# Kernel tuning notes

Hardware: AMD Instinct MI355X
Metric: run time of the kernel (lower is better)

## Reference

```python
import jax, jax.numpy as jnp
import numpy as np

SEQ_LEN = 168; PRED_LEN = 24; N_FEAT = 8; KERNEL = 25
N_QUBITS = 4; N_QLAYERS = 2; CONTEXT = 32; HIDDEN = 8; BATCH = 16384
LAG_POSITIONS = [1, 2, 3, 4, 5, 6, 23, 24, 25, 167, 168]
LAG_IDX = np.array([SEQ_LEN - l for l in LAG_POSITIONS if l <= SEQ_LEN])
N_LAGS = int(LAG_IDX.size)
PI = float(np.pi)


def _apply_1q(state, U, w):
    # apply 2x2 gate U (shared (2,2) or per-sample (B,2,2)) on wire w
    state = jnp.moveaxis(state, 1 + w, -1)
    if U.ndim == 2:
        state = jnp.einsum('ij,b...j->b...i', U, state)
    else:
        state = jnp.einsum('bij,b...j->b...i', U, state)
    return jnp.moveaxis(state, -1, 1 + w)


def _apply_cnot(state, c, t):
    ax_c, ax_t = 1 + c, 1 + t
    s0 = jax.lax.index_in_dim(state, 0, ax_c, keepdims=False)
    s1 = jax.lax.index_in_dim(state, 1, ax_c, keepdims=False)
    s1 = jnp.flip(s1, axis=ax_t - (1 if t > c else 0))
    return jnp.stack([s0, s1], axis=ax_c)


def _ry(theta):  # (B,) -> (B,2,2)
    c, s = jnp.cos(theta / 2), jnp.sin(theta / 2)
    return jnp.stack([jnp.stack([c, -s], -1), jnp.stack([s, c], -1)], -2).astype(jnp.complex64)


def _rot(w):  # w (3,): Rot(phi,theta,omega) = RZ(omega) RY(theta) RZ(phi)
    phi, theta, omega = w[0], w[1], w[2]
    c, s = jnp.cos(theta / 2), jnp.sin(theta / 2)
    ep = jnp.exp(-0.5j * (phi + omega))
    em = jnp.exp(0.5j * (phi - omega))
    return jnp.stack([jnp.stack([ep * c, -em * s]),
                      jnp.stack([jnp.conj(em) * s, jnp.conj(ep) * c])]).astype(jnp.complex64)


def _vqc(inputs, weights):
    # data re-uploading: [RY AngleEmbedding -> Rot per wire -> CNOT ring (range 1)] x N_QLAYERS
    # (StronglyEntanglingLayers is called with 1 layer per upload, so range is always 1)
    B = inputs.shape[0]
    state = jnp.zeros((B,) + (2,) * N_QUBITS, jnp.complex64)
    state = state.at[(slice(None),) + (0,) * N_QUBITS].set(1.0)
    for l in range(N_QLAYERS):
        for q in range(N_QUBITS):
            state = _apply_1q(state, _ry(inputs[:, q]), q)
        for q in range(N_QUBITS):
            state = _apply_1q(state, _rot(weights[l, q]), q)
        for q in range(N_QUBITS):
            state = _apply_cnot(state, q, (q + 1) % N_QUBITS)
    probs = state.real ** 2 + state.imag ** 2  # (B,2,2,2,2)
    zdiag = jnp.array([1.0, -1.0], jnp.float32)
    exps = []
    for q in range(N_QUBITS):
        other = tuple(a for a in range(1, N_QUBITS + 1) if a != 1 + q)
        exps.append(jnp.einsum('bq,q->b', probs.sum(other), zdiag))
    return jnp.stack(exps, axis=-1)  # (B, N_QUBITS)


def _decomp(x, decomp_w):
    # learnable moving-average decomposition (DLinear-style, per-feature softmax kernel, edge padding)
    pad = (KERNEL - 1) // 2
    w = jax.nn.softmax(decomp_w, axis=-1)  # (F,K)
    xp = jnp.pad(x, ((0, 0), (pad, KERNEL - 1 - pad), (0, 0)), mode='edge')
    xc = jnp.moveaxis(xp, 1, 2)  # (B,F,S+K-1)
    trend = jax.lax.conv_general_dilated(xc, w[:, None, :], (1,), 'VALID',
                                         feature_group_count=N_FEAT,
                                         dimension_numbers=('NCH', 'OIH', 'NCH'))
    trend = jnp.moveaxis(trend, 1, 2)  # (B,S,F)
    return x - trend, trend


def forward(x, decomp_w, trend_w, trend_b, seasonal_w, seasonal_b, h0_w, h0_b,
            ta_w, ta_b, sc_w, sc_b, crz_w, crz_b, cn_w, cn_b,
            vqc_r, vqc_u, vqc_c, expand_w, expand_b, mod_w, mod_b, fusion_alpha):
    seasonal, trend = _decomp(x, decomp_w)
    trend_out = jnp.einsum('bsf,ps->bpf', trend, trend_w) + trend_b[None, :, None]
    seasonal_base = jnp.einsum('bsf,ps->bpf', seasonal, seasonal_w) + seasonal_b[None, :, None]
    lag_vals = x[:, LAG_IDX, -1]  # (B, N_LAGS), demand is last feature
    h0 = jnp.tanh(lag_vals @ h0_w.T + h0_b)  # (B,H)
    ctx = jnp.einsum('bsf,cs->bfc', seasonal, ta_w) + ta_b  # (B,F,C)
    gru_in = jnp.tanh(ctx.reshape(x.shape[0], -1) @ sc_w.T + sc_b)  # (B,H)
    # single-step quantum GRU
    xh = jnp.concatenate([gru_in, h0], axis=1)  # (B,2H)
    rz_in = jnp.tanh(xh @ crz_w.T + crz_b) * PI  # r_in == z_in (same compress in source)
    r = jax.nn.sigmoid(_vqc(rz_in, vqc_r) @ expand_w.T + expand_b)
    z = jax.nn.sigmoid(_vqc(rz_in, vqc_u) @ expand_w.T + expand_b)
    n_in = jnp.tanh(jnp.concatenate([r * h0, gru_in], axis=1) @ cn_w.T + cn_b) * PI
    n = jnp.tanh(_vqc(n_in, vqc_c) @ expand_w.T + expand_b)
    h_new = (1 - z) * n + z * h0
    modulation = jnp.tanh(h_new @ mod_w.T + mod_b)  # (B,P)
    seasonal_out = seasonal_base * (1.0 + modulation[:, :, None])
    alpha = jax.nn.sigmoid(fusion_alpha)[0]
    return alpha * seasonal_out + (1 - alpha) * trend_out  # (B,P,F)


def setup_inputs() -> dict:
    key = jax.random.key(0)
    ks = iter(jax.random.split(key, 32))

    def lin(out_d, in_d):
        lim = 1.0 / np.sqrt(in_d)
        return (jax.random.uniform(next(ks), (out_d, in_d), jnp.float32, -lim, lim),
                jax.random.uniform(next(ks), (out_d,), jnp.float32, -lim, lim))

    trend_w, trend_b = lin(PRED_LEN, SEQ_LEN)
    seasonal_w, seasonal_b = lin(PRED_LEN, SEQ_LEN)
    h0_w, h0_b = lin(HIDDEN, N_LAGS)
    ta_w, ta_b = lin(CONTEXT, SEQ_LEN)
    sc_w, sc_b = lin(HIDDEN, N_FEAT * CONTEXT)
    crz_w, crz_b = lin(N_QUBITS, 2 * HIDDEN)
    cn_w, cn_b = lin(N_QUBITS, 2 * HIDDEN)
    expand_w, expand_b = lin(HIDDEN, N_QUBITS)
    mod_w, mod_b = lin(PRED_LEN, HIDDEN)
    return {
        'x': jax.random.normal(next(ks), (BATCH, SEQ_LEN, N_FEAT), jnp.float32),
        'decomp_w': 0.02 * jax.random.normal(next(ks), (N_FEAT, KERNEL), jnp.float32),
        'trend_w': trend_w, 'trend_b': trend_b,
        'seasonal_w': seasonal_w, 'seasonal_b': seasonal_b,
        'h0_w': h0_w, 'h0_b': h0_b,
        'ta_w': ta_w, 'ta_b': ta_b,
        'sc_w': sc_w, 'sc_b': sc_b,
        'crz_w': crz_w, 'crz_b': crz_b,
        'cn_w': cn_w, 'cn_b': cn_b,
        'vqc_r': jax.random.uniform(next(ks), (N_QLAYERS, N_QUBITS, 3), jnp.float32, 0.0, 2 * PI),
        'vqc_u': jax.random.uniform(next(ks), (N_QLAYERS, N_QUBITS, 3), jnp.float32, 0.0, 2 * PI),
        'vqc_c': jax.random.uniform(next(ks), (N_QLAYERS, N_QUBITS, 3), jnp.float32, 0.0, 2 * PI),
        'expand_w': expand_w, 'expand_b': expand_b,
        'mod_w': mod_w, 'mod_b': mod_b,
        'fusion_alpha': jnp.array([0.5], jnp.float32),
    }


def reference(x, decomp_w, trend_w, trend_b, seasonal_w, seasonal_b, h0_w, h0_b,
              ta_w, ta_b, sc_w, sc_b, crz_w, crz_b, cn_w, cn_b,
              vqc_r, vqc_u, vqc_c, expand_w, expand_b, mod_w, mod_b, fusion_alpha):
    return forward(x, decomp_w, trend_w, trend_b, seasonal_w, seasonal_b, h0_w, h0_b,
                   ta_w, ta_b, sc_w, sc_b, crz_w, crz_b, cn_w, cn_b,
                   vqc_r, vqc_u, vqc_c, expand_w, expand_b, mod_w, mod_b, fusion_alpha)
```

## Files before the change

### kernel.cpp

```cpp
#include <hip/hip_runtime.h>
#include <hip/hip_bf16.h>
#include <cmath>

#define SEQ   168
#define NF    8
#define PRED  24
#define HID   8
#define KTOT  1344
#define NSCH  6
#define PI_F  3.14159265358979323846f

#define WS_ROTC     256
#define WS_CGIN     512
#define WS_WT       1024
#define WS_IMG_BYTE 524288

typedef __attribute__((ext_vector_type(8))) short bf16x8;
typedef __attribute__((ext_vector_type(4))) float f32x4;

__device__ __forceinline__ float frcp(float x)  { return __builtin_amdgcn_rcpf(x); }
__device__ __forceinline__ float ftanh(float x) {
    float xc = fminf(fmaxf(x, -15.f), 15.f);
    float e  = __expf(2.f * xc);
    return (e - 1.f) * frcp(e + 1.f);
}
__device__ __forceinline__ float sigm(float x) { return frcp(1.f + __expf(-x)); }
__device__ __forceinline__ unsigned short f2bf(float f) {
    __hip_bfloat16 h = __float2bfloat16(f);
    return __builtin_bit_cast(unsigned short, h);
}
__device__ __forceinline__ unsigned pack2(float a, float b) {
    return (unsigned)f2bf(a) | ((unsigned)f2bf(b) << 16);
}

__global__ void k_compose(const float* __restrict__ decomp_w,
                          const float* __restrict__ trend_w,
                          const float* __restrict__ seasonal_w,
                          const float* __restrict__ ta_w,
                          float* __restrict__ Wt) {
    __shared__ float dwsh[NF * 25];
    int t = threadIdx.x;
    if (t < NF) {
        const float* row = decomp_w + t * 25;
        float m = row[0];
        for (int k = 1; k < 25; ++k) m = fmaxf(m, row[k]);
        float e[25]; float sum = 0.f;
        for (int k = 0; k < 25; ++k) { e[k] = expf(row[k] - m); sum += e[k]; }
        float inv = 1.f / sum;
        for (int k = 0; k < 25; ++k) dwsh[t * 25 + k] = e[k] * inv;
    }
    __syncthreads();
    int n = blockIdx.x * 256 + t;
    if (n >= SEQ * 640) return;
    int sx  = n / 640;
    int col = n % 640;
    int j = col >> 3;
    int f = col & 7;
    const float* dwf = dwsh + f * 25;
    const float* wsel;
    int isTrend = 0;
    if (j < 24)      { wsel = trend_w    + j        * SEQ; isTrend = 1; }
    else if (j < 48) { wsel = seasonal_w + (j - 24) * SEQ; }
    else             { wsel = ta_w       + (j - 48) * SEQ; }
    float acc = 0.f;
    if (sx == 0) {
        for (int s = 0; s <= 12; ++s) {
            float cw = 0.f;
            for (int k = 0; k <= 12 - s; ++k) cw += dwf[k];
            acc = fmaf(cw, wsel[s], acc);
        }
    } else if (sx == 167) {
        for (int s = 155; s < 168; ++s) {
            float cw = 0.f;
            for (int k = 179 - s; k < 25; ++k) cw += dwf[k];
            acc = fmaf(cw, wsel[s], acc);
        }
    } else {
        int lo = sx - 12; if (lo < 0) lo = 0;
        int hi = sx + 12; if (hi > 167) hi = 167;
        for (int s = lo; s <= hi; ++s) acc = fmaf(dwf[sx - s + 12], wsel[s], acc);
    }
    Wt[sx * 640 + col] = isTrend ? acc : (wsel[sx] - acc);
}

__global__ void k_img(const float* __restrict__ Wt, const float* __restrict__ sc_w,
                      const float* __restrict__ h0_w,
                      const float* __restrict__ vr, const float* __restrict__ vu,
                      const float* __restrict__ vc,
                      const float* __restrict__ sc_b, const float* __restrict__ ta_b,
                      float* __restrict__ rotc, float* __restrict__ cgin,
                      unsigned char* __restrict__ imgb) {
    int idx = blockIdx.x * 256 + threadIdx.x;
    if (idx < 12288) {
        int lane = idx & 63;
        int rest = idx >> 6;
        int ks = rest % 6;
        int fc = rest / 6;
        int cf = fc & 3, f = fc >> 2;
        int lr = lane & 15, lg = lane >> 4;
        unsigned short vals[8];
        #pragma unroll
        for (int e = 0; e < 8; ++e) {
            int k = ks * 32 + lg * 8 + e;
            float val = 0.f;
            if (k < SEQ) {
                if (cf < 3) {
                    int col = cf * 16 + lr;
                    val = Wt[k * 640 + (col & 1) * 192 + (col >> 1) * 8 + f];
                } else if (lr < 8) {
                    float a = 0.f;
                    for (int cc = 0; cc < 32; ++cc)
                        a = fmaf(sc_w[lr * 256 + f * 32 + cc], Wt[k * 640 + 384 + cc * 8 + f], a);
                    val = a;
                } else if (f == 7) {
                    const int LIDX[11] = {167,166,165,164,163,162,145,144,143,1,0};
                    #pragma unroll
                    for (int i = 0; i < 11; ++i)
                        if (k == LIDX[i]) val = h0_w[(lr - 8) * 11 + i];
                }
            }
            vals[e] = f2bf(val);
        }
        uint4 o;
        o.x = (unsigned)vals[0] | ((unsigned)vals[1] << 16);
        o.y = (unsigned)vals[2] | ((unsigned)vals[3] << 16);
        o.z = (unsigned)vals[4] | ((unsigned)vals[5] << 16);
        o.w = (unsigned)vals[6] | ((unsigned)vals[7] << 16);
        *(uint4*)(imgb + (size_t)rest * 1024 + lane * 16) = o;
    } else if (blockIdx.x == 48) {
        int t = threadIdx.x;
        if (t >= 64 && t < 88) {
            int n = t - 64;
            int v = n / 8, rest = n % 8;
            const float* w = (v == 0 ? vr : (v == 1 ? vu : vc)) + rest * 3;
            float phi = w[0], th = w[1], om = w[2];
            float c = cosf(0.5f * th), s = sinf(0.5f * th);
            float ap = -0.5f * (phi + om);
            float am =  0.5f * (phi - om);
            float* o = rotc + n * 4;
            o[0] = cosf(ap) * c;
            o[1] = sinf(ap) * c;
            o[2] = cosf(am) * s;
            o[3] = sinf(am) * s;
        } else if (t >= 96 && t < 104) {
            int h = t - 96;
            float a = sc_b[h];
            for (int cc = 0; cc < 32; ++cc) {
                float s = 0.f;
                for (int f = 0; f < 8; ++f) s += sc_w[h * 256 + f * 32 + cc];
                a = fmaf(ta_b[cc], s, a);
            }
            cgin[h] = a;
        }
    }
}

__device__ __forceinline__ float shflg(float v, int grp, int idx) {
    return __shfl(v, grp + idx, 64);
}

__device__ void vqc_run(const float cq[4], const float sq[4],
                        const float* __restrict__ rc,
                        int l, int grp, float exps[4]) {
    float re = (l == 0) ? 1.f : 0.f;
    float im = 0.f;
    #pragma unroll
    for (int layer = 0; layer < 2; ++layer) {
        #pragma unroll
        for (int q = 0; q < 4; ++q) {
            int m = 1 << (3 - q);
            float pre = shflg(re, grp, l ^ m);
            float pim = shflg(im, grp, l ^ m);
            float sg = (l & m) ? sq[q] : -sq[q];
            re = cq[q] * re + sg * pre;
            im = cq[q] * im + sg * pim;
        }
        #pragma unroll
        for (int q = 0; q < 4; ++q) {
            int m = 1 << (3 - q);
            const float* g = rc + (layer * 4 + q) * 4;
            float A = g[0], B = g[1], C = g[2], D = g[3];
            float pre = shflg(re, grp, l ^ m);
            float pim = shflg(im, grp, l ^ m);
            float car, cai, cpr, cpi;
            if (l & m) { car = A; cai = -B; cpr =  C; cpi = -D; }
            else       { car = A; cai =  B; cpr = -C; cpi = -D; }
            float nre = car * re - cai * im + cpr * pre - cpi * pim;
            float nim = car * im + cai * re + cpr * pim + cpi * pre;
            re = nre; im = nim;
        }
        #pragma unroll
        for (int q = 0; q < 4; ++q) {
            int mc = 1 << (3 - q);
            int mt = 1 << (3 - ((q + 1) & 3));
            float pre = shflg(re, grp, l ^ mt);
            float pim = shflg(im, grp, l ^ mt);
            if (l & mc) { re = pre; im = pim; }
        }
    }
    float prob = re * re + im * im;
    float v0 = (l & 8) ? -prob : prob;
    float v1 = (l & 4) ? -prob : prob;
    float v2 = (l & 2) ? -prob : prob;
    float v3 = (l & 1) ? -prob : prob;
    #pragma unroll
    for (int m = 1; m < 16; m <<= 1) {
        v0 += __shfl_xor(v0, m, 64);
        v1 += __shfl_xor(v1, m, 64);
        v2 += __shfl_xor(v2, m, 64);
        v3 += __shfl_xor(v3, m, 64);
    }
    exps[0] = v0; exps[1] = v1; exps[2] = v2; exps[3] = v3;
}

__global__ __launch_bounds__(512, 4)
void k_fused(const float* __restrict__ x, const unsigned char* __restrict__ img,
             const float* __restrict__ rotc, const float* __restrict__ cgin,
             const float* __restrict__ h0_b,
             const float* __restrict__ crz_w, const float* __restrict__ crz_b,
             const float* __restrict__ cn_w, const float* __restrict__ cn_b,
             const float* __restrict__ expand_w, const float* __restrict__ expand_b,
             const float* __restrict__ mod_w, const float* __restrict__ mod_b,
             const float* __restrict__ trend_b, const float* __restrict__ seasonal_b,
             const float* __restrict__ fusion_alpha,
             float* __restrict__ out, int Btot)
{
    __shared__ unsigned char lds[49152];
    float* ghpart = (float*)(lds + 32768);
    float* ghbuf  = (float*)lds;
    float* modt   = (float*)(lds + 2304);

    const int t    = threadIdx.x;
    const int b0   = blockIdx.x * 32;
    const int w    = t >> 6, lane = t & 63, lr = lane & 15, lg = lane >> 4;

    const int arow  = t >> 4;
    const int spair = t & 15;
    int gr = b0 + arow; if (gr >= Btot) gr = Btot - 1;
    const float* xrow = x + (size_t)gr * KTOT;

    const unsigned char* ib = img + (size_t)(w * 24) * 1024 + (size_t)lane * 16;

    float4 raA[4], raB[4];
    #pragma unroll
    for (int u = 0; u < 4; ++u) raA[u] = *(const float4*)&xrow[spair * 16 + u * 4];
    #pragma unroll
    for (int u = 0; u < 4; ++u) raB[u] = *(const float4*)&xrow[256 + spair * 16 + u * 4];
    bf16x8 BrA[4], BrB[4];
    #pragma unroll
    for (int cf = 0; cf < 4; ++cf) BrA[cf] = *(const bf16x8*)&ib[(cf * 6 + 0) * 1024];
    #pragma unroll
    for (int cf = 0; cf < 4; ++cf) BrB[cf] = *(const bf16x8*)&ib[(cf * 6 + 1) * 1024];

    f32x4 acc[3][2], accg[2];
    #pragma unroll
    for (int cf = 0; cf < 3; ++cf) {
        acc[cf][0] = (f32x4){0.f, 0.f, 0.f, 0.f};
        acc[cf][1] = (f32x4){0.f, 0.f, 0.f, 0.f};
    }
    accg[0] = (f32x4){0.f, 0.f, 0.f, 0.f};
    accg[1] = (f32x4){0.f, 0.f, 0.f, 0.f};

    const int wb   = (arow * 64 + spair * 4) ^ ((arow & 7) << 4);
    const int ar0  = (lr * 64 + lg * 16) ^ ((lr & 7) << 4);
    const int ar1  = ((lr + 16) * 64 + lg * 16) ^ ((lr & 7) << 4);

    #pragma unroll
    for (int kc = 0; kc < NSCH; ++kc) {
        const int bufo = (kc & 1) * 16384;
        {
            const float* rf = (kc & 1) ? (const float*)raB : (const float*)raA;
            #pragma unroll
            for (int f = 0; f < 8; ++f)
                *(unsigned*)&lds[bufo + f * 2048 + wb] = pack2(rf[f], rf[8 + f]);
        }
        if (kc + 2 < NSCH) {
            int off = (kc + 2) * 256 + spair * 16;
            if (off > KTOT - 16) off = KTOT - 16;
            if (kc & 1) {
                #pragma unroll
                for (int u = 0; u < 4; ++u) raB[u] = *(const float4*)&xrow[off + u * 4];
            } else {
                #pragma unroll
                for (int u = 0; u < 4; ++u) raA[u] = *(const float4*)&xrow[off + u * 4];
            }
        }
        __syncthreads();
        {
            bf16x8 a0 = *(const bf16x8*)&lds[bufo + w * 2048 + ar0];
            bf16x8 a1 = *(const bf16x8*)&lds[bufo + w * 2048 + ar1];
            if (kc & 1) {
                #pragma unroll
                for (int cf = 0; cf < 3; ++cf) {
                    acc[cf][0] = __builtin_amdgcn_mfma_f32_16x16x32_bf16(a0, BrB[cf], acc[cf][0], 0, 0, 0);
                    acc[cf][1] = __builtin_amdgcn_mfma_f32_16x16x32_bf16(a1, BrB[cf], acc[cf][1], 0, 0, 0);
                }
                accg[0] = __builtin_amdgcn_mfma_f32_16x16x32_bf16(a0, BrB[3], accg[0], 0, 0, 0);
                accg[1] = __builtin_amdgcn_mfma_f32_16x16x32_bf16(a1, BrB[3], accg[1], 0, 0, 0);
            } else {
                #pragma unroll
                for (int cf = 0; cf < 3; ++cf) {
                    acc[cf][0] = __builtin_amdgcn_mfma_f32_16x16x32_bf16(a0, BrA[cf], acc[cf][0], 0, 0, 0);
                    acc[cf][1] = __builtin_amdgcn_mfma_f32_16x16x32_bf16(a1, BrA[cf], acc[cf][1], 0, 0, 0);
                }
                accg[0] = __builtin_amdgcn_mfma_f32_16x16x32_bf16(a0, BrA[3], accg[0], 0, 0, 0);
                accg[1] = __builtin_amdgcn_mfma_f32_16x16x32_bf16(a1, BrA[3], accg[1], 0, 0, 0);
            }
        }
        if (kc + 2 < NSCH) {
            if (kc & 1) {
                #pragma unroll
                for (int cf = 0; cf < 4; ++cf) BrB[cf] = *(const bf16x8*)&ib[(cf * 6 + kc + 2) * 1024];
            } else {
                #pragma unroll
                for (int cf = 0; cf < 4; ++cf) BrA[cf] = *(const bf16x8*)&ib[(cf * 6 + kc + 2) * 1024];
            }
        }
    }

    #pragma unroll
    for (int mf = 0; mf < 2; ++mf)
        #pragma unroll
        for (int reg = 0; reg < 4; ++reg)
            ghpart[(w * 32 + mf * 16 + lg * 4 + reg) * 16 + lr] = accg[mf][reg];
    __syncthreads();
    {
        int row = t >> 4, col = t & 15;
        float s = 0.f;
        #pragma unroll
        for (int f = 0; f < 8; ++f) s += ghpart[f * 512 + row * 16 + col];
        ghbuf[row * 17 + col] = s;
    }
    __syncthreads();

    {
        const int rl  = t >> 4;
        const int l   = t & 15;
        const int grp = lane & 48;
        float gin[HID], h0v[HID];
        #pragma unroll
        for (int h = 0; h < HID; ++h) {
            gin[h] = ftanh(ghbuf[rl * 17 + h]     + cgin[h]);
            h0v[h] = ftanh(ghbuf[rl * 17 + 8 + h] + h0_b[h]);
        }
        float rz[4];
        #pragma unroll
        for (int q = 0; q < 4; ++q) {
            float a = crz_b[q];
            #pragma unroll
            for (int k = 0; k < 8; ++k) a = fmaf(gin[k], crz_w[q * 16 + k], a);
            #pragma unroll
            for (int k = 0; k < 8; ++k) a = fmaf(h0v[k], crz_w[q * 16 + 8 + k], a);
            rz[q] = ftanh(a) * PI_F;
        }
        float cq[4], sq[4];
        #pragma unroll
        for (int q = 0; q < 4; ++q) { cq[q] = __cosf(0.5f * rz[q]); sq[q] = __sinf(0.5f * rz[q]); }

        float er[4], ez[4];
        vqc_run(cq, sq, rotc + 0 * 32, l, grp, er);
        vqc_run(cq, sq, rotc + 1 * 32, l, grp, ez);

        float rr[HID], zz[HID];
        #pragma unroll
        for (int h = 0; h < HID; ++h) {
            float a = expand_b[h], b = expand_b[h];
            #pragma unroll
            for (int q = 0; q < 4; ++q) {
                a = fmaf(er[q], expand_w[h * 4 + q], a);
                b = fmaf(ez[q], expand_w[h * 4 + q], b);
            }
            rr[h] = sigm(a);
            zz[h] = sigm(b);
        }
        float ni[4];
        #pragma unroll
        for (int q = 0; q < 4; ++q) {
            float a = cn_b[q];
            #pragma unroll
            for (int k = 0; k < 8; ++k) a = fmaf(rr[k] * h0v[k], cn_w[q * 16 + k], a);
            #pragma unroll
            for (int k = 0; k < 8; ++k) a = fmaf(gin[k], cn_w[q * 16 + 8 + k], a);
            ni[q] = ftanh(a) * PI_F;
        }
        #pragma unroll
        for (int q = 0; q < 4; ++q) { cq[q] = __cosf(0.5f * ni[q]); sq[q] = __sinf(0.5f * ni[q]); }
        float en[4];
        vqc_run(cq, sq, rotc + 2 * 32, l, grp, en);

        float hn[HID];
        #pragma unroll
        for (int h = 0; h < HID; ++h) {
            float a = expand_b[h];
            #pragma unroll
            for (int q = 0; q < 4; ++q) a = fmaf(en[q], expand_w[h * 4 + q], a);
            float nn = ftanh(a);
            hn[h] = (1.f - zz[h]) * nn + zz[h] * h0v[h];
        }
        int pp = l;
        float a = mod_b[pp];
        #pragma unroll
        for (int h = 0; h < HID; ++h) a = fmaf(hn[h], mod_w[pp * 8 + h], a);
        modt[rl * 25 + pp] = ftanh(a);
        if (l < 8) {
            pp = l + 16;
            a = mod_b[pp];
            #pragma unroll
            for (int h = 0; h < HID; ++h) a = fmaf(hn[h], mod_w[pp * 8 + h], a);
            modt[rl * 25 + pp] = ftanh(a);
        }
    }
    __syncthreads();

    const float alpha = sigm(fusion_alpha[0]);
    #pragma unroll
    for (int cf = 0; cf < 3; ++cf) {
        int p = cf * 8 + (lr >> 1);
        float tb = trend_b[p], sb = seasonal_b[p];
        #pragma unroll
        for (int mf = 0; mf < 2; ++mf) {
            #pragma unroll
            for (int reg = 0; reg < 4; ++reg) {
                int rl = mf * 16 + lg * 4 + reg;
                float v  = acc[cf][mf][reg];
                float pt = __shfl_xor(v, 1, 64);
                if (!(lr & 1)) {
                    int R = b0 + rl;
                    if (R < Btot) {
                        float md = modt[rl * 25 + p];
                        float res = alpha * ((pt + sb) * (1.f + md))
                                  + (1.f - alpha) * (v + tb);
                        out[(size_t)R * 192 + p * 8 + w] = res;
                    }
                }
            }
        }
    }
}

extern "C" void kernel_launch(void* const* d_in, const int* in_sizes, int n_in,
                              void* d_out, int out_size, void* d_ws, size_t ws_size,
                              hipStream_t stream) {
    const float* x          = (const float*)d_in[0];
    const float* decomp_w   = (const float*)d_in[1];
    const float* trend_w    = (const float*)d_in[2];
    const float* trend_b    = (const float*)d_in[3];
    const float* seasonal_w = (const float*)d_in[4];
    const float* seasonal_b = (const float*)d_in[5];
    const float* h0_w       = (const float*)d_in[6];
    const float* h0_b       = (const float*)d_in[7];
    const float* ta_w       = (const float*)d_in[8];
    const float* ta_b       = (const float*)d_in[9];
    const float* sc_w       = (const float*)d_in[10];
    const float* sc_b       = (const float*)d_in[11];
    const float* crz_w      = (const float*)d_in[12];
    const float* crz_b      = (const float*)d_in[13];
    const float* cn_w       = (const float*)d_in[14];
    const float* cn_b       = (const float*)d_in[15];
    const float* vqc_r      = (const float*)d_in[16];
    const float* vqc_u      = (const float*)d_in[17];
    const float* vqc_c      = (const float*)d_in[18];
    const float* expand_w   = (const float*)d_in[19];
    const float* expand_b   = (const float*)d_in[20];
    const float* mod_w      = (const float*)d_in[21];
    const float* mod_b      = (const float*)d_in[22];
    const float* fus_a      = (const float*)d_in[23];
    float* out = (float*)d_out;

    float* ws   = (float*)d_ws;
    float* rotc = ws + WS_ROTC;
    float* cgin = ws + WS_CGIN;
    float* Wt   = ws + WS_WT;
    unsigned char* img = (unsigned char*)d_ws + WS_IMG_BYTE;

    const int Btot = in_sizes[0] / (SEQ * NF);

    k_compose<<<(SEQ * 640 + 255) / 256, 256, 0, stream>>>(decomp_w, trend_w, seasonal_w, ta_w, Wt);
    k_img<<<49, 256, 0, stream>>>(Wt, sc_w, h0_w, vqc_r, vqc_u, vqc_c, sc_b, ta_b,
                                  rotc, cgin, img);

    k_fused<<<(Btot + 31) / 32, 512, 0, stream>>>(x, img, rotc, cgin, h0_b,
                                                  crz_w, crz_b, cn_w, cn_b,
                                                  expand_w, expand_b, mod_w, mod_b,
                                                  trend_b, seasonal_b, fus_a, out, Btot);
}
```

Baseline: 55.06 us.

## Split fused kernel into MFMA GEMM kernel and separate post-processing kernel

The single fused kernel is split in two. One kernel runs only the bf16 MFMA projection and writes a per-row 400-float intermediate (trend, seasonal and gate pre-activations) to workspace. A second 256-thread kernel reloads that intermediate and performs the VQC simulation, gating, modulation and output fusion with coalesced writes. The weight image column mapping is reordered so trend and seasonal columns are contiguous, and the GEMM launch bound drops from 4 to 2 blocks per CU. The intent is to decouple the serial VQC epilogue from the memory-bound GEMM. In exchange it adds a large intermediate write and read plus an extra launch.

```diff
diff --git a/kernel.cpp b/kernel.cpp
--- a/kernel.cpp
+++ b/kernel.cpp
@@ -13,6 +13,7 @@
 #define WS_ROTC     256
 #define WS_CGIN     512
 #define WS_WT       1024
+#define WS_Y        400000
 #define WS_IMG_BYTE 524288
 
 typedef __attribute__((ext_vector_type(8))) short bf16x8;
@@ -105,8 +106,10 @@
             float val = 0.f;
             if (k < SEQ) {
                 if (cf < 3) {
-                    int col = cf * 16 + lr;
-                    val = Wt[k * 640 + (col & 1) * 192 + (col >> 1) * 8 + f];
+                    int c = cf * 16 + lr;
+                    int ts = (c >= 24);
+                    int p  = ts ? (c - 24) : c;
+                    val = Wt[k * 640 + ts * 192 + p * 8 + f];
                 } else if (lr < 8) {
                     float a = 0.f;
                     for (int cc = 0; cc < 32; ++cc)
@@ -155,80 +158,12 @@
     }
 }
 
-__device__ __forceinline__ float shflg(float v, int grp, int idx) {
-    return __shfl(v, grp + idx, 64);
-}
-
-__device__ void vqc_run(const float cq[4], const float sq[4],
-                        const float* __restrict__ rc,
-                        int l, int grp, float exps[4]) {
-    float re = (l == 0) ? 1.f : 0.f;
-    float im = 0.f;
-    #pragma unroll
-    for (int layer = 0; layer < 2; ++layer) {
-        #pragma unroll
-        for (int q = 0; q < 4; ++q) {
-            int m = 1 << (3 - q);
-            float pre = shflg(re, grp, l ^ m);
-            float pim = shflg(im, grp, l ^ m);
-            float sg = (l & m) ? sq[q] : -sq[q];
-            re = cq[q] * re + sg * pre;
-            im = cq[q] * im + sg * pim;
-        }
-        #pragma unroll
-        for (int q = 0; q < 4; ++q) {
-            int m = 1 << (3 - q);
-            const float* g = rc + (layer * 4 + q) * 4;
-            float A = g[0], B = g[1], C = g[2], D = g[3];
-            float pre = shflg(re, grp, l ^ m);
-            float pim = shflg(im, grp, l ^ m);
-            float car, cai, cpr, cpi;
-            if (l & m) { car = A; cai = -B; cpr =  C; cpi = -D; }
-            else       { car = A; cai =  B; cpr = -C; cpi = -D; }
-            float nre = car * re - cai * im + cpr * pre - cpi * pim;
-            float nim = car * im + cai * re + cpr * pim + cpi * pre;
-            re = nre; im = nim;
-        }
-        #pragma unroll
-        for (int q = 0; q < 4; ++q) {
-            int mc = 1 << (3 - q);
-            int mt = 1 << (3 - ((q + 1) & 3));
-            float pre = shflg(re, grp, l ^ mt);
-            float pim = shflg(im, grp, l ^ mt);
-            if (l & mc) { re = pre; im = pim; }
-        }
-    }
-    float prob = re * re + im * im;
-    float v0 = (l & 8) ? -prob : prob;
-    float v1 = (l & 4) ? -prob : prob;
-    float v2 = (l & 2) ? -prob : prob;
-    float v3 = (l & 1) ? -prob : prob;
-    #pragma unroll
-    for (int m = 1; m < 16; m <<= 1) {
-        v0 += __shfl_xor(v0, m, 64);
-        v1 += __shfl_xor(v1, m, 64);
-        v2 += __shfl_xor(v2, m, 64);
-        v3 += __shfl_xor(v3, m, 64);
-    }
-    exps[0] = v0; exps[1] = v1; exps[2] = v2; exps[3] = v3;
-}
-
-__global__ __launch_bounds__(512, 4)
-void k_fused(const float* __restrict__ x, const unsigned char* __restrict__ img,
-             const float* __restrict__ rotc, const float* __restrict__ cgin,
-             const float* __restrict__ h0_b,
-             const float* __restrict__ crz_w, const float* __restrict__ crz_b,
-             const float* __restrict__ cn_w, const float* __restrict__ cn_b,
-             const float* __restrict__ expand_w, const float* __restrict__ expand_b,
-             const float* __restrict__ mod_w, const float* __restrict__ mod_b,
-             const float* __restrict__ trend_b, const float* __restrict__ seasonal_b,
-             const float* __restrict__ fusion_alpha,
-             float* __restrict__ out, int Btot)
+__global__ __launch_bounds__(512, 2)
+void k_gemm(const float* __restrict__ x, const unsigned char* __restrict__ img,
+            float* __restrict__ y, int Btot)
 {
     __shared__ unsigned char lds[49152];
     float* ghpart = (float*)(lds + 32768);
-    float* ghbuf  = (float*)lds;
-    float* modt   = (float*)(lds + 2304);
 
     const int t    = threadIdx.x;
     const int b0   = blockIdx.x * 32;
@@ -238,7 +173,6 @@
     const int spair = t & 15;
     int gr = b0 + arow; if (gr >= Btot) gr = Btot - 1;
     const float* xrow = x + (size_t)gr * KTOT;
-
     const unsigned char* ib = img + (size_t)(w * 24) * 1024 + (size_t)lane * 16;
 
     float4 raA[4], raB[4];
@@ -319,6 +253,20 @@
     }
 
     #pragma unroll
+    for (int cf = 0; cf < 3; ++cf) {
+        int c = cf * 16 + lr;
+        int base = (c < 24) ? (w * 24 + c) : (192 + w * 24 + (c - 24));
+        #pragma unroll
+        for (int mf = 0; mf < 2; ++mf) {
+            #pragma unroll
+            for (int reg = 0; reg < 4; ++reg) {
+                int R = b0 + mf * 16 + lg * 4 + reg;
+                if (R < Btot) y[(size_t)R * 400 + base] = (mf ? acc[cf][1][reg] : acc[cf][0][reg]);
+            }
+        }
+    }
+
+    #pragma unroll
     for (int mf = 0; mf < 2; ++mf)
         #pragma unroll
         for (int reg = 0; reg < 4; ++reg)
@@ -329,19 +277,106 @@
         float s = 0.f;
         #pragma unroll
         for (int f = 0; f < 8; ++f) s += ghpart[f * 512 + row * 16 + col];
-        ghbuf[row * 17 + col] = s;
+        int R = b0 + row;
+        if (R < Btot) y[(size_t)R * 400 + 384 + col] = s;
+    }
+}
+
+__device__ __forceinline__ float shflg(float v, int grp, int idx) {
+    return __shfl(v, grp + idx, 64);
+}
+
+__device__ void vqc_run(const float cq[4], const float sq[4],
+                        const float* __restrict__ rc,
+                        int l, int grp, float exps[4]) {
+    float re = (l == 0) ? 1.f : 0.f;
+    float im = 0.f;
+    #pragma unroll
+    for (int layer = 0; layer < 2; ++layer) {
+        #pragma unroll
+        for (int q = 0; q < 4; ++q) {
+            int m = 1 << (3 - q);
+            float pre = shflg(re, grp, l ^ m);
+            float pim = shflg(im, grp, l ^ m);
+            float sg = (l & m) ? sq[q] : -sq[q];
+            re = cq[q] * re + sg * pre;
+            im = cq[q] * im + sg * pim;
+        }
+        #pragma unroll
+        for (int q = 0; q < 4; ++q) {
+            int m = 1 << (3 - q);
+            const float* g = rc + (layer * 4 + q) * 4;
+            float A = g[0], B = g[1], C = g[2], D = g[3];
+            float pre = shflg(re, grp, l ^ m);
+            float pim = shflg(im, grp, l ^ m);
+            float car, cai, cpr, cpi;
+            if (l & m) { car = A; cai = -B; cpr =  C; cpi = -D; }
+            else       { car = A; cai =  B; cpr = -C; cpi = -D; }
+            float nre = car * re - cai * im + cpr * pre - cpi * pim;
+            float nim = car * im + cai * re + cpr * pim + cpi * pre;
+            re = nre; im = nim;
+        }
+        #pragma unroll
+        for (int q = 0; q < 4; ++q) {
+            int mc = 1 << (3 - q);
+            int mt = 1 << (3 - ((q + 1) & 3));
+            float pre = shflg(re, grp, l ^ mt);
+            float pim = shflg(im, grp, l ^ mt);
+            if (l & mc) { re = pre; im = pim; }
+        }
+    }
+    float prob = re * re + im * im;
+    float v0 = (l & 8) ? -prob : prob;
+    float v1 = (l & 4) ? -prob : prob;
+    float v2 = (l & 2) ? -prob : prob;
+    float v3 = (l & 1) ? -prob : prob;
+    #pragma unroll
+    for (int m = 1; m < 16; m <<= 1) {
+        v0 += __shfl_xor(v0, m, 64);
+        v1 += __shfl_xor(v1, m, 64);
+        v2 += __shfl_xor(v2, m, 64);
+        v3 += __shfl_xor(v3, m, 64);
+    }
+    exps[0] = v0; exps[1] = v1; exps[2] = v2; exps[3] = v3;
+}
+
+__global__ __launch_bounds__(256)
+void k_post(const float* __restrict__ y, const float* __restrict__ rotc,
+            const float* __restrict__ cgin, const float* __restrict__ h0_b,
+            const float* __restrict__ crz_w, const float* __restrict__ crz_b,
+            const float* __restrict__ cn_w, const float* __restrict__ cn_b,
+            const float* __restrict__ expand_w, const float* __restrict__ expand_b,
+            const float* __restrict__ mod_w, const float* __restrict__ mod_b,
+            const float* __restrict__ trend_b, const float* __restrict__ seasonal_b,
+            const float* __restrict__ fusion_alpha,
+            float* __restrict__ out, int Btot)
+{
+    __shared__ float yb[16 * 400];
+    __shared__ float modt[16 * 25];
+    const int t  = threadIdx.x;
+    const int b0 = blockIdx.x * 16;
+
+    #pragma unroll
+    for (int i = 0; i < 7; ++i) {
+        int idx = t + i * 256;
+        if (idx < 1600) {
+            int r = idx / 100, cu = idx % 100;
+            int R = b0 + r; if (R >= Btot) R = Btot - 1;
+            *(float4*)&yb[r * 400 + cu * 4] = *(const float4*)&y[(size_t)R * 400 + cu * 4];
+        }
     }
     __syncthreads();
 
     {
         const int rl  = t >> 4;
         const int l   = t & 15;
+        const int lane = t & 63;
         const int grp = lane & 48;
         float gin[HID], h0v[HID];
         #pragma unroll
         for (int h = 0; h < HID; ++h) {
-            gin[h] = ftanh(ghbuf[rl * 17 + h]     + cgin[h]);
-            h0v[h] = ftanh(ghbuf[rl * 17 + 8 + h] + h0_b[h]);
+            gin[h] = ftanh(yb[rl * 400 + 384 + h] + cgin[h]);
+            h0v[h] = ftanh(yb[rl * 400 + 392 + h] + h0_b[h]);
         }
         float rz[4];
         #pragma unroll
@@ -414,26 +449,17 @@
 
     const float alpha = sigm(fusion_alpha[0]);
     #pragma unroll
-    for (int cf = 0; cf < 3; ++cf) {
-        int p = cf * 8 + (lr >> 1);
-        float tb = trend_b[p], sb = seasonal_b[p];
-        #pragma unroll
-        for (int mf = 0; mf < 2; ++mf) {
-            #pragma unroll
-            for (int reg = 0; reg < 4; ++reg) {
-                int rl = mf * 16 + lg * 4 + reg;
-                float v  = acc[cf][mf][reg];
-                float pt = __shfl_xor(v, 1, 64);
-                if (!(lr & 1)) {
-                    int R = b0 + rl;
-                    if (R < Btot) {
-                        float md = modt[rl * 25 + p];
-                        float res = alpha * ((pt + sb) * (1.f + md))
-                                  + (1.f - alpha) * (v + tb);
-                        out[(size_t)R * 192 + p * 8 + w] = res;
-                    }
-                }
-            }
+    for (int i = 0; i < 12; ++i) {
+        int idx = t + i * 256;
+        int r = idx / 192, o = idx % 192;
+        int R = b0 + r;
+        if (R < Btot) {
+            int p = o >> 3, f = o & 7;
+            float T = yb[r * 400 + f * 24 + p];
+            float S = yb[r * 400 + 192 + f * 24 + p];
+            float md = modt[r * 25 + p];
+            out[(size_t)R * 192 + o] = alpha * ((S + seasonal_b[p]) * (1.f + md))
+                                     + (1.f - alpha) * (T + trend_b[p]);
         }
     }
 }
@@ -471,6 +497,7 @@
     float* rotc = ws + WS_ROTC;
     float* cgin = ws + WS_CGIN;
     float* Wt   = ws + WS_WT;
+    float* y    = ws + WS_Y;
     unsigned char* img = (unsigned char*)d_ws + WS_IMG_BYTE;
 
     const int Btot = in_sizes[0] / (SEQ * NF);
@@ -479,8 +506,10 @@
     k_img<<<49, 256, 0, stream>>>(Wt, sc_w, h0_w, vqc_r, vqc_u, vqc_c, sc_b, ta_b,
                                   rotc, cgin, img);
 
-    k_fused<<<(Btot + 31) / 32, 512, 0, stream>>>(x, img, rotc, cgin, h0_b,
-                                                  crz_w, crz_b, cn_w, cn_b,
-                                                  expand_w, expand_b, mod_w, mod_b,
-                                                  trend_b, seasonal_b, fus_a, out, Btot);
-}
+    k_gemm<<<(Btot + 31) / 32, 512, 0, stream>>>(x, img, y, Btot);
+
+    k_post<<<(Btot + 15) / 16, 256, 0, stream>>>(y, rotc, cgin, h0_b,
+                                                 crz_w, crz_b, cn_w, cn_b,
+                                                 expand_w, expand_b, mod_w, mod_b,
+                                                 trend_b, seasonal_b, fus_a, out, Btot);
+}
```

Result: slower. 60.63 us (+10.1%).
